# Performance work log

Measured on AMD Instinct MI355X. Metric: run time of the kernel, lower is better.

## Reference

```python
import jax, jax.numpy as jnp
import numpy as np

BN_EPS = 1e-5


def setup_inputs() -> dict:
    key = jax.random.key(0)
    k1, k2, k3 = jax.random.split(key, 3)
    B, IN, H, C = 65536, 784, 1024, 10
    x = jax.random.normal(k1, (B, IN), dtype=jnp.float32)
    # Kaiming-ish real-valued latent weights
    w1 = jax.random.normal(k2, (H, IN), dtype=jnp.float32) * 0.03
    w2 = jax.random.normal(k3, (C, H), dtype=jnp.float32) * 0.03
    gamma = jnp.ones((H,), dtype=jnp.float32)
    beta = jnp.zeros((H,), dtype=jnp.float32)
    return {"x": x, "w1": w1, "w2": w2, "gamma": gamma, "beta": beta}


def _bin_weight(w):
    # XNOR-Net weight binarization: per-output-row alpha * sign(w)
    alpha = jnp.mean(jnp.abs(w), axis=1, keepdims=True)  # [out, 1]
    return alpha * jnp.sign(w)


def reference(x, w1, w2, gamma, beta):
    x = x.reshape(x.shape[0], -1)                      # [B, 784]
    h = x @ _bin_weight(w1).T                          # [B, 1024]
    # BatchNorm1d, training mode: batch mean / biased variance
    mu = jnp.mean(h, axis=0)
    var = jnp.mean(jnp.square(h - mu), axis=0)
    h = gamma * (h - mu) * jax.lax.rsqrt(var + BN_EPS) + beta
    a = jnp.sign(h)                                    # binarized activation
    out = a @ _bin_weight(w2).T                        # [B, 10]
    return out
```

## Files before the change

### kernel.cpp

```cpp
#include <hip/hip_runtime.h>
#include <hip/hip_fp16.h>

#define BATCH   65536
#define IN_DIM  784
#define KPAD    800
#define K2      1600
#define H_DIM   1024
#define C_DIM   10
#define BN_EPS  1e-5f
#define NT      (K2 / 32)

typedef _Float16 half8 __attribute__((ext_vector_type(8)));
typedef _Float16 half4 __attribute__((ext_vector_type(4)));
typedef float    f32x4 __attribute__((ext_vector_type(4)));

#if defined(__has_builtin)
#if __has_builtin(__builtin_amdgcn_global_load_lds)
#define HAVE_ASYNC 1
#endif
#endif
#ifndef HAVE_ASYNC
#define HAVE_ASYNC 0
#endif

__device__ __forceinline__ void stage16(const _Float16* g, _Float16* ldsBase, int lane) {
#if HAVE_ASYNC
  __builtin_amdgcn_global_load_lds((const __attribute__((address_space(1))) void*)g,
                                   (__attribute__((address_space(3))) void*)ldsBase,
                                   16, 0, 0);
#else
  *(half8*)(ldsBase + lane * 8) = *(const half8*)g;
#endif
}

__global__ __launch_bounds__(256) void split_x(const float* __restrict__ x,
                                               _Float16* __restrict__ X2) {
  const long tid = (long)blockIdx.x * 256 + threadIdx.x;
  const long row = tid / 200;
  const int  q   = (int)(tid - row * 200);
  const int  k   = q * 4;
  half4 hi = {}, lo = {};
  if (k < IN_DIM) {
    const f32x4 v = *(const f32x4*)&x[row * IN_DIM + k];
#pragma unroll
    for (int i = 0; i < 4; ++i) {
      const _Float16 h = (_Float16)v[i];
      hi[i] = h;
      lo[i] = (_Float16)(v[i] - (float)h);
    }
  }
  _Float16* dst = X2 + row * K2 + k;
  *(half4*)dst = hi;
  *(half4*)(dst + KPAD) = lo;
}

__global__ __launch_bounds__(256) void prep_w(const float* __restrict__ w1,
                                              const float* __restrict__ w2,
                                              float* __restrict__ alpha1,
                                              _Float16* __restrict__ S2,
                                              float* __restrict__ bw2) {
  __shared__ float red[4];
  const int tid = threadIdx.x, lane = tid & 63, wave = tid >> 6;
  const int j = blockIdx.x;
  if (j < H_DIM) {
    const float* wr = w1 + (long)j * IN_DIM;
    float s = 0.f;
    for (int k = tid; k < IN_DIM; k += 256) s += fabsf(wr[k]);
#pragma unroll
    for (int off = 32; off > 0; off >>= 1) s += __shfl_xor(s, off, 64);
    if (lane == 0) red[wave] = s;
    __syncthreads();
    if (tid == 0) alpha1[j] = (red[0] + red[1] + red[2] + red[3]) * (1.f / IN_DIM);
    _Float16* dr = S2 + (long)j * K2;
    for (int k = tid; k < KPAD; k += 256) {
      const float v = (k < IN_DIM) ? wr[k] : 0.f;
      const _Float16 sg = (_Float16)((v > 0.f) ? 1.f : ((v < 0.f) ? -1.f : 0.f));
      dr[k] = sg;
      dr[KPAD + k] = sg;
    }
  } else {
    const int c = j - H_DIM;
    const float* wr = w2 + (long)c * H_DIM;
    float s = 0.f;
    for (int k = tid; k < H_DIM; k += 256) s += fabsf(wr[k]);
#pragma unroll
    for (int off = 32; off > 0; off >>= 1) s += __shfl_xor(s, off, 64);
    if (lane == 0) red[wave] = s;
    __syncthreads();
    const float alpha = (red[0] + red[1] + red[2] + red[3]) * (1.f / H_DIM);
    for (int k = tid; k < H_DIM; k += 256) {
      const float v = wr[k];
      const float sg = (v > 0.f) ? 1.f : ((v < 0.f) ? -1.f : 0.f);
      bw2[(long)c * H_DIM + k] = alpha * sg;
    }
  }
}

__global__ __launch_bounds__(512, 2) void gemm1(const _Float16* __restrict__ X2,
                                                const _Float16* __restrict__ S2,
                                                const float* __restrict__ alpha1,
                                                float* __restrict__ H,
                                                float* __restrict__ colsum,
                                                float* __restrict__ colsumsq) {
  __shared__ _Float16 lds[5 * 16384];
  const int tid  = threadIdx.x;
  const int lane = tid & 63;
  const int w    = tid >> 6;
  const int wr   = w >> 2;
  const int wc   = w & 3;

  const int b     = blockIdx.x;
  const int xcd   = b & 7;
  const int local = b >> 3;
  const long m0   = (long)(xcd * 32 + (local >> 2)) * 256;
  const int  n0   = (local & 3) * 256;

  const int c8 = ((lane & 3) ^ ((lane >> 3) & 3)) * 8;
  const _Float16* aG = X2 + (m0 + w * 32 + (lane >> 2)) * K2 + c8;
  const _Float16* bG = S2 + (long)(n0 + w * 32 + (lane >> 2)) * K2 + c8;
  const int ldsW0 = (w * 32) * 32;
  const int ldsW1 = (w * 32 + 16) * 32;

  const int fr = lane & 15;
  const int kc = lane >> 4;
  const int cp = (kc ^ ((fr >> 1) & 3)) * 8;
  const int aoff = (wr * 128 + fr) * 32 + cp;
  const int boff = (wc * 64 + fr) * 32 + cp;

  f32x4 acc[8][4] = {};

#pragma unroll
  for (int kt = 0; kt < 4; ++kt) {
    _Float16* Ap = &lds[kt * 16384];
    _Float16* Bp = Ap + 8192;
    stage16(aG + kt * 32, Ap + ldsW0, lane);
    stage16(aG + 16 * K2 + kt * 32, Ap + ldsW1, lane);
    stage16(bG + kt * 32, Bp + ldsW0, lane);
    stage16(bG + 16 * K2 + kt * 32, Bp + ldsW1, lane);
  }

  int scur = 0;
  int spre = 4;
  for (int t = 0; t < NT; ++t) {
    _Float16* Asl = &lds[scur * 16384];
    _Float16* Bsl = Asl + 8192;
    const int ks = (t + 4 < NT) ? (t + 4) * 32 : (NT - 1) * 32;
    _Float16* Ap = &lds[spre * 16384];
    _Float16* Bp = Ap + 8192;

    asm volatile("s_waitcnt vmcnt(12)" ::: "memory");
    __builtin_amdgcn_s_barrier();
    asm volatile("" ::: "memory");

    stage16(aG + ks, Ap + ldsW0, lane);
    stage16(aG + 16 * K2 + ks, Ap + ldsW1, lane);
    half8 af[4], bf[4];
#pragma unroll
    for (int ni = 0; ni < 4; ++ni) bf[ni] = *(const half8*)&Bsl[boff + ni * 512];
#pragma unroll
    for (int mi = 0; mi < 4; ++mi) af[mi] = *(const half8*)&Asl[aoff + mi * 512];
    __builtin_amdgcn_s_setprio(1);
#pragma unroll
    for (int mi = 0; mi < 4; ++mi)
#pragma unroll
      for (int ni = 0; ni < 4; ++ni)
        acc[mi][ni] = __builtin_amdgcn_mfma_f32_16x16x32_f16(af[mi], bf[ni], acc[mi][ni], 0, 0, 0);
    __builtin_amdgcn_s_setprio(0);
    __builtin_amdgcn_s_barrier();

    stage16(bG + ks, Bp + ldsW0, lane);
    stage16(bG + 16 * K2 + ks, Bp + ldsW1, lane);
#pragma unroll
    for (int mi = 0; mi < 4; ++mi) af[mi] = *(const half8*)&Asl[aoff + (mi + 4) * 512];
    __builtin_amdgcn_s_setprio(1);
#pragma unroll
    for (int mi = 0; mi < 4; ++mi)
#pragma unroll
      for (int ni = 0; ni < 4; ++ni)
        acc[mi + 4][ni] = __builtin_amdgcn_mfma_f32_16x16x32_f16(af[mi], bf[ni], acc[mi + 4][ni], 0, 0, 0);
    __builtin_amdgcn_s_setprio(0);

    scur = (scur == 4) ? 0 : scur + 1;
    spre = (spre == 4) ? 0 : spre + 1;
  }

  asm volatile("s_waitcnt vmcnt(0)" ::: "memory");

  const int rq = (lane >> 4) * 4;
#pragma unroll
  for (int ni = 0; ni < 4; ++ni) {
    const int col = n0 + wc * 64 + ni * 16 + fr;
    const float a1 = alpha1[col];
    float s = 0.f, q = 0.f;
#pragma unroll
    for (int mi = 0; mi < 8; ++mi) {
#pragma unroll
      for (int r = 0; r < 4; ++r) {
        const long row = m0 + wr * 128 + mi * 16 + rq + r;
        const float v = acc[mi][ni][r] * a1;
        H[row * H_DIM + col] = v;
        s += v;
        q += v * v;
      }
    }
    s += __shfl_xor(s, 16, 64);
    s += __shfl_xor(s, 32, 64);
    q += __shfl_xor(q, 16, 64);
    q += __shfl_xor(q, 32, 64);
    if ((lane >> 4) == 0) {
      atomicAdd(&colsum[col], s);
      atomicAdd(&colsumsq[col], q);
    }
  }
}

__global__ __launch_bounds__(256, 2) void final_k(const float* __restrict__ H,
                                                  const float* __restrict__ colsum,
                                                  const float* __restrict__ colsumsq,
                                                  const float* __restrict__ gamma,
                                                  const float* __restrict__ beta,
                                                  const float* __restrict__ bw2,
                                                  float* __restrict__ out) {
  const int tid = threadIdx.x, lane = tid & 63, wave = tid >> 6;
  f32x4 w2r[4][C_DIM];
  f32x4 csr[4], tsr[4];
#pragma unroll
  for (int c4 = 0; c4 < 4; ++c4) {
    const int col = c4 * 256 + lane * 4;
    const f32x4 s  = *(const f32x4*)&colsum[col];
    const f32x4 q  = *(const f32x4*)&colsumsq[col];
    const f32x4 g  = *(const f32x4*)&gamma[col];
    const f32x4 bt = *(const f32x4*)&beta[col];
    f32x4 c, t;
#pragma unroll
    for (int i = 0; i < 4; ++i) {
      const float mu  = s[i] * (1.f / BATCH);
      const float var = q[i] * (1.f / BATCH) - mu * mu;
      c[i] = g[i] * rsqrtf(var + BN_EPS);
      t[i] = bt[i] - c[i] * mu;
    }
    csr[c4] = c;
    tsr[c4] = t;
#pragma unroll
    for (int oc = 0; oc < C_DIM; ++oc)
      w2r[c4][oc] = *(const f32x4*)&bw2[oc * H_DIM + col];
  }

  const long wrow0 = ((long)blockIdx.x * 4 + wave) * 8;
#pragma unroll 1
  for (int r = 0; r < 8; ++r) {
    const long row = wrow0 + r;
    const float* hr = H + row * H_DIM;
    f32x4 h[4];
#pragma unroll
    for (int c4 = 0; c4 < 4; ++c4) h[c4] = *(const f32x4*)&hr[c4 * 256 + lane * 4];
    float p[C_DIM] = {};
#pragma unroll
    for (int c4 = 0; c4 < 4; ++c4) {
      f32x4 a;
#pragma unroll
      for (int i = 0; i < 4; ++i) {
        const float hv = h[c4][i] * csr[c4][i] + tsr[c4][i];
        a[i] = (hv > 0.f) ? 1.f : ((hv < 0.f) ? -1.f : 0.f);
      }
#pragma unroll
      for (int oc = 0; oc < C_DIM; ++oc) {
        const f32x4 wv = w2r[c4][oc];
        p[oc] += a[0] * wv[0] + a[1] * wv[1] + a[2] * wv[2] + a[3] * wv[3];
      }
    }
#pragma unroll
    for (int oc = 0; oc < C_DIM; ++oc) {
#pragma unroll
      for (int off = 32; off > 0; off >>= 1) p[oc] += __shfl_xor(p[oc], off, 64);
    }
    if (lane == 0) {
#pragma unroll
      for (int oc = 0; oc < C_DIM; ++oc) out[row * C_DIM + oc] = p[oc];
    }
  }
}

extern "C" void kernel_launch(void* const* d_in, const int* in_sizes, int n_in,
                              void* d_out, int out_size, void* d_ws, size_t ws_size,
                              hipStream_t stream) {
  const float* x     = (const float*)d_in[0];
  const float* w1    = (const float*)d_in[1];
  const float* w2    = (const float*)d_in[2];
  const float* gamma = (const float*)d_in[3];
  const float* beta  = (const float*)d_in[4];
  float* out = (float*)d_out;

  char* ws = (char*)d_ws;
  _Float16* X2     = (_Float16*)(ws + 0);
  float*    H      = (float*)  (ws + 209715200LL);
  _Float16* S2     = (_Float16*)(ws + 478150656LL);
  float*    BW2    = (float*)  (ws + 481427456LL);
  float*    ALPHA1 = (float*)  (ws + 481468416LL);
  float*    COLS   = (float*)  (ws + 481472512LL);
  float*    COLQ   = (float*)  (ws + 481476608LL);

  hipMemsetAsync(COLS, 0, 2 * H_DIM * sizeof(float), stream);
  split_x<<<(BATCH * 200) / 256, 256, 0, stream>>>(x, X2);
  prep_w<<<H_DIM + C_DIM, 256, 0, stream>>>(w1, w2, ALPHA1, S2, BW2);
  gemm1<<<1024, 512, 0, stream>>>(X2, S2, ALPHA1, H, COLS, COLQ);
  final_k<<<BATCH / 32, 256, 0, stream>>>(H, COLS, COLQ, gamma, beta, BW2, out);
}
```

Baseline: 615.0 us.

## Reuse one sign-weight tile for both hi and lo halves of split-fp16 GEMM

The GEMM used to treat the hi/lo fp16 split of x as a K=1600 reduction against a duplicated sign-weight matrix. Now each k-step stages the hi and lo A-tiles plus a single B-tile of K=800, and applies the same B fragments to both halves. This halves B-side global and LDS traffic and removes the duplicated S2 storage. It also changes the LDS pipeline from 5 stages to 3 larger stages, and split_x now writes 8-wide vectors per thread. The cost is more A registers per step (8 fragments) and a shallower prefetch depth.

```diff
diff --git a/kernel.cpp b/kernel.cpp
--- a/kernel.cpp
+++ b/kernel.cpp
@@ -5,10 +5,11 @@
 #define IN_DIM  784
 #define KPAD    800
 #define K2      1600
+#define KH      800
+#define NSTEP   25
 #define H_DIM   1024
 #define C_DIM   10
 #define BN_EPS  1e-5f
-#define NT      (K2 / 32)
 
 typedef _Float16 half8 __attribute__((ext_vector_type(8)));
 typedef _Float16 half4 __attribute__((ext_vector_type(4)));
@@ -36,22 +37,25 @@
 __global__ __launch_bounds__(256) void split_x(const float* __restrict__ x,
                                                _Float16* __restrict__ X2) {
   const long tid = (long)blockIdx.x * 256 + threadIdx.x;
-  const long row = tid / 200;
-  const int  q   = (int)(tid - row * 200);
-  const int  k   = q * 4;
-  half4 hi = {}, lo = {};
+  const long row = tid / 100;
+  const int  q   = (int)(tid - row * 100);
+  const int  k   = q * 8;
+  half8 hi = {}, lo = {};
   if (k < IN_DIM) {
-    const f32x4 v = *(const f32x4*)&x[row * IN_DIM + k];
-#pragma unroll
-    for (int i = 0; i < 4; ++i) {
-      const _Float16 h = (_Float16)v[i];
-      hi[i] = h;
-      lo[i] = (_Float16)(v[i] - (float)h);
+#pragma unroll
+    for (int h4 = 0; h4 < 2; ++h4) {
+      const f32x4 v = *(const f32x4*)&x[row * IN_DIM + k + h4 * 4];
+#pragma unroll
+      for (int i = 0; i < 4; ++i) {
+        const _Float16 h = (_Float16)v[i];
+        hi[h4 * 4 + i] = h;
+        lo[h4 * 4 + i] = (_Float16)(v[i] - (float)h);
+      }
     }
   }
   _Float16* dst = X2 + row * K2 + k;
-  *(half4*)dst = hi;
-  *(half4*)(dst + KPAD) = lo;
+  *(half8*)dst = hi;
+  *(half8*)(dst + KPAD) = lo;
 }
 
 __global__ __launch_bounds__(256) void prep_w(const float* __restrict__ w1,
@@ -71,12 +75,10 @@
     if (lane == 0) red[wave] = s;
     __syncthreads();
     if (tid == 0) alpha1[j] = (red[0] + red[1] + red[2] + red[3]) * (1.f / IN_DIM);
-    _Float16* dr = S2 + (long)j * K2;
-    for (int k = tid; k < KPAD; k += 256) {
+    _Float16* dr = S2 + (long)j * KH;
+    for (int k = tid; k < KH; k += 256) {
       const float v = (k < IN_DIM) ? wr[k] : 0.f;
-      const _Float16 sg = (_Float16)((v > 0.f) ? 1.f : ((v < 0.f) ? -1.f : 0.f));
-      dr[k] = sg;
-      dr[KPAD + k] = sg;
+      dr[k] = (_Float16)((v > 0.f) ? 1.f : ((v < 0.f) ? -1.f : 0.f));
     }
   } else {
     const int c = j - H_DIM;
@@ -102,7 +104,7 @@
                                                 float* __restrict__ H,
                                                 float* __restrict__ colsum,
                                                 float* __restrict__ colsumsq) {
-  __shared__ _Float16 lds[5 * 16384];
+  __shared__ _Float16 lds[3 * 24576];
   const int tid  = threadIdx.x;
   const int lane = tid & 63;
   const int w    = tid >> 6;
@@ -117,7 +119,7 @@
 
   const int c8 = ((lane & 3) ^ ((lane >> 3) & 3)) * 8;
   const _Float16* aG = X2 + (m0 + w * 32 + (lane >> 2)) * K2 + c8;
-  const _Float16* bG = S2 + (long)(n0 + w * 32 + (lane >> 2)) * K2 + c8;
+  const _Float16* bG = S2 + (long)(n0 + w * 32 + (lane >> 2)) * KH + c8;
   const int ldsW0 = (w * 32) * 32;
   const int ldsW1 = (w * 32 + 16) * 32;
 
@@ -130,58 +132,60 @@
   f32x4 acc[8][4] = {};
 
 #pragma unroll
-  for (int kt = 0; kt < 4; ++kt) {
-    _Float16* Ap = &lds[kt * 16384];
-    _Float16* Bp = Ap + 8192;
-    stage16(aG + kt * 32, Ap + ldsW0, lane);
-    stage16(aG + 16 * K2 + kt * 32, Ap + ldsW1, lane);
-    stage16(bG + kt * 32, Bp + ldsW0, lane);
-    stage16(bG + 16 * K2 + kt * 32, Bp + ldsW1, lane);
+  for (int kt = 0; kt < 2; ++kt) {
+    _Float16* S = &lds[kt * 24576];
+    const int k0 = kt * 32;
+    stage16(aG + k0,                  S + ldsW0, lane);
+    stage16(aG + 16 * K2 + k0,        S + ldsW1, lane);
+    stage16(aG + KPAD + k0,           S + 8192 + ldsW0, lane);
+    stage16(aG + KPAD + 16 * K2 + k0, S + 8192 + ldsW1, lane);
+    stage16(bG + k0,                  S + 16384 + ldsW0, lane);
+    stage16(bG + 16 * KH + k0,        S + 16384 + ldsW1, lane);
   }
 
   int scur = 0;
-  int spre = 4;
-  for (int t = 0; t < NT; ++t) {
-    _Float16* Asl = &lds[scur * 16384];
-    _Float16* Bsl = Asl + 8192;
-    const int ks = (t + 4 < NT) ? (t + 4) * 32 : (NT - 1) * 32;
-    _Float16* Ap = &lds[spre * 16384];
-    _Float16* Bp = Ap + 8192;
-
-    asm volatile("s_waitcnt vmcnt(12)" ::: "memory");
+  int spre = 2;
+  for (int t = 0; t < NSTEP; ++t) {
+    _Float16* S = &lds[scur * 24576];
+    const int ks = (t + 2 < NSTEP) ? (t + 2) * 32 : (NSTEP - 1) * 32;
+    _Float16* P = &lds[spre * 24576];
+
+    asm volatile("s_waitcnt vmcnt(6)" ::: "memory");
     __builtin_amdgcn_s_barrier();
     asm volatile("" ::: "memory");
 
-    stage16(aG + ks, Ap + ldsW0, lane);
-    stage16(aG + 16 * K2 + ks, Ap + ldsW1, lane);
-    half8 af[4], bf[4];
-#pragma unroll
-    for (int ni = 0; ni < 4; ++ni) bf[ni] = *(const half8*)&Bsl[boff + ni * 512];
-#pragma unroll
-    for (int mi = 0; mi < 4; ++mi) af[mi] = *(const half8*)&Asl[aoff + mi * 512];
+    stage16(aG + ks,                  P + ldsW0, lane);
+    stage16(aG + 16 * K2 + ks,        P + ldsW1, lane);
+    stage16(aG + KPAD + ks,           P + 8192 + ldsW0, lane);
+    stage16(aG + KPAD + 16 * K2 + ks, P + 8192 + ldsW1, lane);
+    half8 af[8], bf[4];
+#pragma unroll
+    for (int ni = 0; ni < 4; ++ni) bf[ni] = *(const half8*)&S[16384 + boff + ni * 512];
+#pragma unroll
+    for (int mi = 0; mi < 8; ++mi) af[mi] = *(const half8*)&S[aoff + mi * 512];
     __builtin_amdgcn_s_setprio(1);
 #pragma unroll
-    for (int mi = 0; mi < 4; ++mi)
+    for (int mi = 0; mi < 8; ++mi)
 #pragma unroll
       for (int ni = 0; ni < 4; ++ni)
         acc[mi][ni] = __builtin_amdgcn_mfma_f32_16x16x32_f16(af[mi], bf[ni], acc[mi][ni], 0, 0, 0);
     __builtin_amdgcn_s_setprio(0);
     __builtin_amdgcn_s_barrier();
 
-    stage16(bG + ks, Bp + ldsW0, lane);
-    stage16(bG + 16 * K2 + ks, Bp + ldsW1, lane);
-#pragma unroll
-    for (int mi = 0; mi < 4; ++mi) af[mi] = *(const half8*)&Asl[aoff + (mi + 4) * 512];
+    stage16(bG + ks,           P + 16384 + ldsW0, lane);
+    stage16(bG + 16 * KH + ks, P + 16384 + ldsW1, lane);
+#pragma unroll
+    for (int mi = 0; mi < 8; ++mi) af[mi] = *(const half8*)&S[8192 + aoff + mi * 512];
     __builtin_amdgcn_s_setprio(1);
 #pragma unroll
-    for (int mi = 0; mi < 4; ++mi)
+    for (int mi = 0; mi < 8; ++mi)
 #pragma unroll
       for (int ni = 0; ni < 4; ++ni)
-        acc[mi + 4][ni] = __builtin_amdgcn_mfma_f32_16x16x32_f16(af[mi], bf[ni], acc[mi + 4][ni], 0, 0, 0);
+        acc[mi][ni] = __builtin_amdgcn_mfma_f32_16x16x32_f16(af[mi], bf[ni], acc[mi][ni], 0, 0, 0);
     __builtin_amdgcn_s_setprio(0);
 
-    scur = (scur == 4) ? 0 : scur + 1;
-    spre = (spre == 4) ? 0 : spre + 1;
+    scur = (scur == 2) ? 0 : scur + 1;
+    spre = (spre == 2) ? 0 : spre + 1;
   }
 
   asm volatile("s_waitcnt vmcnt(0)" ::: "memory");
@@ -301,7 +305,7 @@
   float*    COLQ   = (float*)  (ws + 481476608LL);
 
   hipMemsetAsync(COLS, 0, 2 * H_DIM * sizeof(float), stream);
-  split_x<<<(BATCH * 200) / 256, 256, 0, stream>>>(x, X2);
+  split_x<<<(BATCH * 100) / 256, 256, 0, stream>>>(x, X2);
   prep_w<<<H_DIM + C_DIM, 256, 0, stream>>>(w1, w2, ALPHA1, S2, BW2);
   gemm1<<<1024, 512, 0, stream>>>(X2, S2, ALPHA1, H, COLS, COLQ);
   final_k<<<BATCH / 32, 256, 0, stream>>>(H, COLS, COLQ, gamma, beta, BW2, out);
```

Result: no change. 606.5 us (-1.4%).
